# Kernel tuning notes

Measured on AMD Instinct MI355X. Metric: run time of the kernel, lower is better.

Reference implementation:

```python
import jax, jax.numpy as jnp
import numpy as np

B, L, H, NH = 8, 1024, 1024, 16
HD = H // NH  # head_dim = 64
SCALE = HD ** -0.5


def setup_inputs() -> dict:
    key = jax.random.key(0)
    kx, kqkv, kw, kb = jax.random.split(key, 4)
    x = jax.random.normal(kx, (B, L, H), dtype=jnp.float32)
    # nn.Linear(H, 3H, bias=False): weight [3H, H]
    w_qkv = jax.random.normal(kqkv, (3 * H, H), dtype=jnp.float32) * (H ** -0.5)
    # out_proj: nn.Linear(H, H) with bias
    w_out = jax.random.normal(kw, (H, H), dtype=jnp.float32) * (H ** -0.5)
    b_out = jax.random.normal(kb, (H,), dtype=jnp.float32) * 0.01
    return {"x": x, "w_qkv": w_qkv, "w_out": w_out, "b_out": b_out}


def reference(x, w_qkv, w_out, b_out):
    # qkv projection: [B, L, 3H]
    qkv = jnp.einsum('bld,ed->ble', x, w_qkv)
    # rearrange 'b l (qkv h d) -> qkv b h l d'
    qkv = qkv.reshape(B, L, 3, NH, HD)
    q = qkv[:, :, 0].transpose(0, 2, 1, 3)  # [B, NH, L, HD]
    k = qkv[:, :, 1].transpose(0, 2, 1, 3)
    v = qkv[:, :, 2].transpose(0, 2, 1, 3)
    att = jnp.einsum('bhxd,bhyd->bhxy', q, k) * SCALE
    att = jax.nn.softmax(att, axis=-1)
    o = jnp.einsum('bhxy,bhyd->bhxd', att, v)  # [B, NH, L, HD]
    o = o.transpose(0, 2, 1, 3).reshape(B, L, H)
    return jnp.einsum('bld,ed->ble', o, w_out) + b_out
```

## Files before the change

kernel.cpp:

```cpp
#include <hip/hip_runtime.h>


typedef short s16x8 __attribute__((ext_vector_type(8)));
typedef float f32x4 __attribute__((ext_vector_type(4)));
typedef unsigned int u32x2 __attribute__((ext_vector_type(2)));
typedef unsigned int u32x4 __attribute__((ext_vector_type(4)));

__device__ __forceinline__ unsigned short f2bf(float f) {
    union { float f; unsigned u; } c; c.f = f;
    return (unsigned short)((c.u + 0x7FFFu + ((c.u >> 16) & 1u)) >> 16);
}
__device__ __forceinline__ unsigned pack2bf(float a, float b) {
    union { float f; unsigned u; } ca, cb; ca.f = a; cb.f = b;
    return __builtin_amdgcn_perm(cb.u + 0x8000u, ca.u + 0x8000u, 0x07060302u);
}

#define GLOAD_LDS(g, l) __builtin_amdgcn_global_load_lds( \
    (const __attribute__((address_space(1))) void*)(g),   \
    (__attribute__((address_space(3))) void*)(l), 16, 0, 0)

__global__ __launch_bounds__(256) void cvt3(
    const float* __restrict__ s0, unsigned short* __restrict__ d0, int n0,
    const float* __restrict__ s1, unsigned short* __restrict__ d1, int n1,
    const float* __restrict__ s2, unsigned short* __restrict__ d2, int n2)
{
    long i = ((long)blockIdx.x * 256 + threadIdx.x) * 8;
    const float* s; unsigned short* d; long off;
    if (i < n0)                  { s = s0; d = d0; off = i; }
    else if (i < (long)n0 + n1)  { s = s1; d = d1; off = i - n0; }
    else                         { s = s2; d = d2; off = i - n0 - n1; }
    f32x4 a = *(const f32x4*)(s + off);
    f32x4 b = *(const f32x4*)(s + off + 4);
    u32x4 r;
    r[0] = pack2bf(a[0], a[1]); r[1] = pack2bf(a[2], a[3]);
    r[2] = pack2bf(b[0], b[1]); r[3] = pack2bf(b[2], b[3]);
    *(u32x4*)(d + off) = r;
}

template<int EPI>
__global__ __launch_bounds__(256) void gemm16(
    const unsigned short* __restrict__ A, const unsigned short* __restrict__ Bm,
    unsigned short* __restrict__ Cq, unsigned short* __restrict__ Cv,
    float* __restrict__ Cf, const float* __restrict__ bias,
    int N, int K)
{
    __shared__ unsigned short As[128 * 32];
    __shared__ unsigned short Bs[128 * 32];
    const int tid = threadIdx.x, lane = tid & 63, wave = tid >> 6;
    const int quad = lane >> 4, l16 = lane & 15;
    const int wm = (wave >> 1) * 64, wn = (wave & 1) * 64;
    const int m0 = blockIdx.y * 128, n0 = blockIdx.x * 128;

    const int lin0 = wave * 128 + lane, lin1 = lin0 + 64;
    const unsigned short* gA0 = A + (size_t)(m0 + (lin0 >> 2)) * K + (lin0 & 3) * 8;
    const unsigned short* gA1 = A + (size_t)(m0 + (lin1 >> 2)) * K + (lin1 & 3) * 8;
    const unsigned short* gB0 = Bm + (size_t)(n0 + (lin0 >> 2)) * K + (lin0 & 3) * 8;
    const unsigned short* gB1 = Bm + (size_t)(n0 + (lin1 >> 2)) * K + (lin1 & 3) * 8;

    f32x4 acc[4][4] = {};
    for (int k0 = 0; k0 < K; k0 += 32) {
        __syncthreads();
        GLOAD_LDS(gA0, As + lin0 * 8);
        GLOAD_LDS(gA1, As + lin1 * 8);
        GLOAD_LDS(gB0, Bs + lin0 * 8);
        GLOAD_LDS(gB1, Bs + lin1 * 8);
        gA0 += 32; gA1 += 32; gB0 += 32; gB1 += 32;
        __syncthreads();
        s16x8 af[4], bf[4];
        #pragma unroll
        for (int i = 0; i < 4; ++i)
            af[i] = *(const s16x8*)(As + (wm + i * 16 + l16) * 32 + quad * 8);
        #pragma unroll
        for (int j = 0; j < 4; ++j)
            bf[j] = *(const s16x8*)(Bs + (wn + j * 16 + l16) * 32 + quad * 8);
        #pragma unroll
        for (int i = 0; i < 4; ++i)
            #pragma unroll
            for (int j = 0; j < 4; ++j)
                acc[i][j] = __builtin_amdgcn_mfma_f32_16x16x32_bf16(af[i], bf[j], acc[i][j], 0, 0, 0);
    }

    if (EPI == 1) {
        #pragma unroll
        for (int j = 0; j < 4; ++j) {
            int col = n0 + wn + j * 16 + l16;
            float bv = bias[col];
            #pragma unroll
            for (int i = 0; i < 4; ++i)
                #pragma unroll
                for (int r = 0; r < 4; ++r)
                    Cf[(size_t)(m0 + wm + i * 16 + quad * 4 + r) * N + col] = acc[i][j][r] + bv;
        }
    } else if (n0 < 2048) {
        #pragma unroll
        for (int j = 0; j < 4; ++j) {
            int col = n0 + wn + j * 16 + l16;
            #pragma unroll
            for (int i = 0; i < 4; ++i)
                #pragma unroll
                for (int r = 0; r < 4; ++r)
                    Cq[(size_t)(m0 + wm + i * 16 + quad * 4 + r) * 2048 + col] = f2bf(acc[i][j][r]);
        }
    } else {
        #pragma unroll
        for (int j = 0; j < 4; ++j) {
            int dcol = n0 + wn + j * 16 + l16 - 2048;
            int hh = dcol >> 6, dd = dcol & 63;
            #pragma unroll
            for (int i = 0; i < 4; ++i)
                #pragma unroll
                for (int r = 0; r < 4; ++r) {
                    int row = m0 + wm + i * 16 + quad * 4 + r;
                    int bb = row >> 10, l = row & 1023;
                    Cv[(size_t)((bb * 16 + hh) * 64 + dd) * 1024 + l] = f2bf(acc[i][j][r]);
                }
        }
    }
}

__global__ __launch_bounds__(256) void attn(
    const unsigned short* __restrict__ qk, const unsigned short* __restrict__ Vt,
    unsigned short* __restrict__ O)
{
    __shared__ unsigned short Qs[64 * 72];
    __shared__ unsigned short Ks[64 * 72];
    __shared__ unsigned short Vs[64 * 72];
    __shared__ unsigned short Ps[4][16 * 72];

    const int bh = blockIdx.y, b = bh >> 4, h = bh & 15;
    const int q0 = blockIdx.x * 64;
    const int tid = threadIdx.x, lane = tid & 63, wave = tid >> 6;
    const int quad = lane >> 4, l16 = lane & 15;

    #pragma unroll
    for (int i = 0; i < 2; ++i) {
        int v = tid + i * 256;
        int l = v >> 3, d0 = (v & 7) * 8;
        *(s16x8*)(Qs + l * 72 + d0) =
            *(const s16x8*)(qk + (size_t)(b * 1024 + q0 + l) * 2048 + h * 64 + d0);
    }
    __syncthreads();
    s16x8 qf[2];
    #pragma unroll
    for (int s = 0; s < 2; ++s)
        qf[s] = *(const s16x8*)(Qs + (wave * 16 + l16) * 72 + s * 32 + quad * 8);

    f32x4 Oacc[4] = {};
    float lsum = 0.0f;

    for (int kv = 0; kv < 1024; kv += 64) {
        __syncthreads();
        #pragma unroll
        for (int i = 0; i < 2; ++i) {
            int v = tid + i * 256;
            int l = v >> 3, d0 = (v & 7) * 8;
            *(s16x8*)(Ks + l * 72 + d0) =
                *(const s16x8*)(qk + (size_t)(b * 1024 + kv + l) * 2048 + 1024 + h * 64 + d0);
            *(s16x8*)(Vs + l * 72 + d0) =
                *(const s16x8*)(Vt + ((size_t)bh * 64 + l) * 1024 + kv + d0);
        }
        __syncthreads();

        f32x4 Sacc[4] = {};
        #pragma unroll
        for (int j = 0; j < 4; ++j) {
            #pragma unroll
            for (int s = 0; s < 2; ++s) {
                s16x8 kf = *(const s16x8*)(Ks + (j * 16 + l16) * 72 + s * 32 + quad * 8);
                Sacc[j] = __builtin_amdgcn_mfma_f32_16x16x32_bf16(kf, qf[s], Sacc[j], 0, 0, 0);
            }
        }

        #pragma unroll
        for (int j = 0; j < 4; ++j) {
            float p0 = __expf(Sacc[j][0] * 0.125f);
            float p1 = __expf(Sacc[j][1] * 0.125f);
            float p2 = __expf(Sacc[j][2] * 0.125f);
            float p3 = __expf(Sacc[j][3] * 0.125f);
            lsum += (p0 + p1) + (p2 + p3);
            u32x2 pw;
            pw[0] = pack2bf(p0, p1);
            pw[1] = pack2bf(p2, p3);
            *(u32x2*)(Ps[wave] + l16 * 72 + j * 16 + quad * 4) = pw;
        }
        asm volatile("s_waitcnt lgkmcnt(0)" ::: "memory");

        #pragma unroll
        for (int s = 0; s < 2; ++s) {
            s16x8 pf = *(const s16x8*)(Ps[wave] + l16 * 72 + s * 32 + quad * 8);
            #pragma unroll
            for (int j = 0; j < 4; ++j) {
                s16x8 vf = *(const s16x8*)(Vs + (j * 16 + l16) * 72 + s * 32 + quad * 8);
                Oacc[j] = __builtin_amdgcn_mfma_f32_16x16x32_bf16(pf, vf, Oacc[j], 0, 0, 0);
            }
        }
    }

    lsum += __shfl_xor(lsum, 16, 64);
    lsum += __shfl_xor(lsum, 32, 64);
    float rinv[4];
    #pragma unroll
    for (int r = 0; r < 4; ++r)
        rinv[r] = 1.0f / __shfl(lsum, quad * 4 + r, 64);

    #pragma unroll
    for (int j = 0; j < 4; ++j)
        #pragma unroll
        for (int r = 0; r < 4; ++r) {
            int row = q0 + wave * 16 + quad * 4 + r;
            int col = h * 64 + j * 16 + l16;
            O[(size_t)(b * 1024 + row) * 1024 + col] = f2bf(Oacc[j][r] * rinv[r]);
        }
}

extern "C" void kernel_launch(void* const* d_in, const int* in_sizes, int n_in,
                              void* d_out, int out_size, void* d_ws, size_t ws_size,
                              hipStream_t stream) {
    const float* x     = (const float*)d_in[0];
    const float* w_qkv = (const float*)d_in[1];
    const float* w_out = (const float*)d_in[2];
    const float* b_out = (const float*)d_in[3];
    float* out = (float*)d_out;

    const int nx = 8192 * 1024, nwq = 3072 * 1024, nwo = 1024 * 1024;
    unsigned short* xb  = (unsigned short*)d_ws;
    unsigned short* wqb = xb + nx;
    unsigned short* wob = wqb + nwq;
    unsigned short* qkb = wob + nwo;
    unsigned short* Vt  = qkb + (size_t)8192 * 2048;
    unsigned short* Ob  = xb;

    dim3 blk(256);
    cvt3<<<6144, blk, 0, stream>>>(x, xb, nx, w_qkv, wqb, nwq, w_out, wob, nwo);
    gemm16<0><<<dim3(24, 64), blk, 0, stream>>>(xb, wqb, qkb, Vt, nullptr, nullptr, 3072, 1024);
    attn<<<dim3(16, 128), blk, 0, stream>>>(qkb, Vt, Ob);
    gemm16<1><<<dim3(8, 64), blk, 0, stream>>>(Ob, wob, nullptr, nullptr, out, b_out, 1024, 1024);
}
```

Baseline: 261.9 us.

## Swizzle LDS layouts and use direct global-to-LDS loads in attention

The GEMM's shared-memory tiles get an XOR swizzle applied on both the global_load_lds write addresses and the fragment reads, to cut LDS bank conflicts. In attention, Q fragments now load straight from global memory into registers, skipping the LDS staging and a barrier. K and V tiles move from register-mediated copies into padded LDS to direct global-to-LDS loads into unpadded, XOR-swizzled tiles. This reduces VGPR traffic and LDS footprint, but leaves the loads unpipelined and makes correctness depend on matching swizzle math.

```diff
diff --git a/kernel.cpp b/kernel.cpp
--- a/kernel.cpp
+++ b/kernel.cpp
@@ -52,10 +52,15 @@
     const int m0 = blockIdx.y * 128, n0 = blockIdx.x * 128;
 
     const int lin0 = wave * 128 + lane, lin1 = lin0 + 64;
-    const unsigned short* gA0 = A + (size_t)(m0 + (lin0 >> 2)) * K + (lin0 & 3) * 8;
-    const unsigned short* gA1 = A + (size_t)(m0 + (lin1 >> 2)) * K + (lin1 & 3) * 8;
-    const unsigned short* gB0 = Bm + (size_t)(n0 + (lin0 >> 2)) * K + (lin0 & 3) * 8;
-    const unsigned short* gB1 = Bm + (size_t)(n0 + (lin1 >> 2)) * K + (lin1 & 3) * 8;
+    const int r0 = lin0 >> 2, r1 = lin1 >> 2;
+    const int q0c = (lin0 & 3) ^ ((r0 >> 1) & 3);
+    const int q1c = (lin1 & 3) ^ ((r1 >> 1) & 3);
+    const unsigned short* gA0 = A + (size_t)(m0 + r0) * K + q0c * 8;
+    const unsigned short* gA1 = A + (size_t)(m0 + r1) * K + q1c * 8;
+    const unsigned short* gB0 = Bm + (size_t)(n0 + r0) * K + q0c * 8;
+    const unsigned short* gB1 = Bm + (size_t)(n0 + r1) * K + q1c * 8;
+
+    const int pc = ((quad ^ ((l16 >> 1) & 3))) * 8;
 
     f32x4 acc[4][4] = {};
     for (int k0 = 0; k0 < K; k0 += 32) {
@@ -69,10 +74,10 @@
         s16x8 af[4], bf[4];
         #pragma unroll
         for (int i = 0; i < 4; ++i)
-            af[i] = *(const s16x8*)(As + (wm + i * 16 + l16) * 32 + quad * 8);
+            af[i] = *(const s16x8*)(As + (wm + i * 16 + l16) * 32 + pc);
         #pragma unroll
         for (int j = 0; j < 4; ++j)
-            bf[j] = *(const s16x8*)(Bs + (wn + j * 16 + l16) * 32 + quad * 8);
+            bf[j] = *(const s16x8*)(Bs + (wn + j * 16 + l16) * 32 + pc);
         #pragma unroll
         for (int i = 0; i < 4; ++i)
             #pragma unroll
@@ -122,9 +127,8 @@
     const unsigned short* __restrict__ qk, const unsigned short* __restrict__ Vt,
     unsigned short* __restrict__ O)
 {
-    __shared__ unsigned short Qs[64 * 72];
-    __shared__ unsigned short Ks[64 * 72];
-    __shared__ unsigned short Vs[64 * 72];
+    __shared__ unsigned short Ks[64 * 64];
+    __shared__ unsigned short Vs[64 * 64];
     __shared__ unsigned short Ps[4][16 * 72];
 
     const int bh = blockIdx.y, b = bh >> 4, h = bh & 15;
@@ -132,33 +136,36 @@
     const int tid = threadIdx.x, lane = tid & 63, wave = tid >> 6;
     const int quad = lane >> 4, l16 = lane & 15;
 
-    #pragma unroll
-    for (int i = 0; i < 2; ++i) {
-        int v = tid + i * 256;
-        int l = v >> 3, d0 = (v & 7) * 8;
-        *(s16x8*)(Qs + l * 72 + d0) =
-            *(const s16x8*)(qk + (size_t)(b * 1024 + q0 + l) * 2048 + h * 64 + d0);
-    }
-    __syncthreads();
+    const unsigned short* qrow = qk + (size_t)(b * 1024 + q0 + wave * 16 + l16) * 2048 + h * 64;
     s16x8 qf[2];
-    #pragma unroll
-    for (int s = 0; s < 2; ++s)
-        qf[s] = *(const s16x8*)(Qs + (wave * 16 + l16) * 72 + s * 32 + quad * 8);
+    qf[0] = *(const s16x8*)(qrow + quad * 8);
+    qf[1] = *(const s16x8*)(qrow + 32 + quad * 8);
+
+    const int rl = lane >> 3;
+    const int qc = (lane & 7) ^ rl;
+    const int g0 = wave * 2, g1 = g0 + 1;
+    const unsigned short* srcK0 = qk + (size_t)(b * 1024 + g0 * 8 + rl) * 2048 + 1024 + h * 64 + qc * 8;
+    const unsigned short* srcK1 = qk + (size_t)(b * 1024 + g1 * 8 + rl) * 2048 + 1024 + h * 64 + qc * 8;
+    const unsigned short* srcV0 = Vt + (size_t)(bh * 64 + g0 * 8 + rl) * 1024 + qc * 8;
+    const unsigned short* srcV1 = Vt + (size_t)(bh * 64 + g1 * 8 + rl) * 1024 + qc * 8;
+    unsigned short* dK0 = Ks + g0 * 512 + lane * 8;
+    unsigned short* dK1 = Ks + g1 * 512 + lane * 8;
+    unsigned short* dV0 = Vs + g0 * 512 + lane * 8;
+    unsigned short* dV1 = Vs + g1 * 512 + lane * 8;
+
+    const int sw = l16 & 7;
 
     f32x4 Oacc[4] = {};
     float lsum = 0.0f;
 
     for (int kv = 0; kv < 1024; kv += 64) {
         __syncthreads();
-        #pragma unroll
-        for (int i = 0; i < 2; ++i) {
-            int v = tid + i * 256;
-            int l = v >> 3, d0 = (v & 7) * 8;
-            *(s16x8*)(Ks + l * 72 + d0) =
-                *(const s16x8*)(qk + (size_t)(b * 1024 + kv + l) * 2048 + 1024 + h * 64 + d0);
-            *(s16x8*)(Vs + l * 72 + d0) =
-                *(const s16x8*)(Vt + ((size_t)bh * 64 + l) * 1024 + kv + d0);
-        }
+        GLOAD_LDS(srcK0, dK0);
+        GLOAD_LDS(srcK1, dK1);
+        GLOAD_LDS(srcV0, dV0);
+        GLOAD_LDS(srcV1, dV1);
+        srcK0 += (size_t)64 * 2048; srcK1 += (size_t)64 * 2048;
+        srcV0 += 64; srcV1 += 64;
         __syncthreads();
 
         f32x4 Sacc[4] = {};
@@ -166,7 +173,7 @@
         for (int j = 0; j < 4; ++j) {
             #pragma unroll
             for (int s = 0; s < 2; ++s) {
-                s16x8 kf = *(const s16x8*)(Ks + (j * 16 + l16) * 72 + s * 32 + quad * 8);
+                s16x8 kf = *(const s16x8*)(Ks + (j * 16 + l16) * 64 + (((s * 4 + quad) ^ sw)) * 8);
                 Sacc[j] = __builtin_amdgcn_mfma_f32_16x16x32_bf16(kf, qf[s], Sacc[j], 0, 0, 0);
             }
         }
@@ -190,7 +197,7 @@
             s16x8 pf = *(const s16x8*)(Ps[wave] + l16 * 72 + s * 32 + quad * 8);
             #pragma unroll
             for (int j = 0; j < 4; ++j) {
-                s16x8 vf = *(const s16x8*)(Vs + (j * 16 + l16) * 72 + s * 32 + quad * 8);
+                s16x8 vf = *(const s16x8*)(Vs + (j * 16 + l16) * 64 + (((s * 4 + quad) ^ sw)) * 8);
                 Oacc[j] = __builtin_amdgcn_mfma_f32_16x16x32_bf16(pf, vf, Oacc[j], 0, 0, 0);
             }
         }
```

Measured after the change: 256.2 us. 1.02x faster.
